# Kernel optimization log

Hardware: AMD Instinct MI355X
Metric: run time of the kernel (lower is better)

The kernel has to match this reference:

```python
import jax, jax.numpy as jnp
import numpy as np

B, T, F, D, H = 16, 512, 32, 256, 256
EPS = 1e-5


def _layernorm(y, g, b):
    m = jnp.mean(y, axis=-1, keepdims=True)
    v = jnp.mean((y - m) ** 2, axis=-1, keepdims=True)
    return (y - m) / jnp.sqrt(v + EPS) * g + b


def setup_inputs() -> dict:
    key = jax.random.key(0)
    ks = jax.random.split(key, 24)
    s = lambda fan_in: 1.0 / np.sqrt(fan_in)
    u = lambda k, shape, fan_in: jax.random.uniform(k, shape, jnp.float32, -s(fan_in), s(fan_in))
    return {
        "x": jax.random.normal(ks[0], (B, T, F), jnp.float32),
        # per-feature Linear(1, D), stacked over F
        "proj_w": u(ks[1], (F, D), 1),
        "proj_b": u(ks[2], (F, D), 1),
        # per-feature scorer GRN(D, H, 1), stacked over F
        "sc_fc1_w": u(ks[3], (F, H, D), D),
        "sc_fc1_b": u(ks[4], (F, H), D),
        "sc_fc2_w": u(ks[5], (F, 1, H), H),
        "sc_fc2_b": u(ks[6], (F, 1), H),
        "sc_gate_w": u(ks[7], (F, 1, 1), 1),
        "sc_gate_b": u(ks[8], (F, 1), 1),
        "sc_skip_w": u(ks[9], (F, 1, D), D),
        "sc_skip_b": u(ks[10], (F, 1), D),
        "sc_ln_g": jnp.ones((F, 1), jnp.float32),
        "sc_ln_b": jnp.zeros((F, 1), jnp.float32),
        # post GRN(D, H, D); in_dim == out_dim -> skip is identity
        "post_fc1_w": u(ks[11], (H, D), D),
        "post_fc1_b": u(ks[12], (H,), D),
        "post_fc2_w": u(ks[13], (D, H), H),
        "post_fc2_b": u(ks[14], (D,), H),
        "post_gate_w": u(ks[15], (D, D), D),
        "post_gate_b": u(ks[16], (D,), D),
        "post_ln_g": jnp.ones((D,), jnp.float32),
        "post_ln_b": jnp.zeros((D,), jnp.float32),
    }


def reference(x, proj_w, proj_b, sc_fc1_w, sc_fc1_b, sc_fc2_w, sc_fc2_b,
              sc_gate_w, sc_gate_b, sc_skip_w, sc_skip_b, sc_ln_g, sc_ln_b,
              post_fc1_w, post_fc1_b, post_fc2_w, post_fc2_b,
              post_gate_w, post_gate_b, post_ln_g, post_ln_b):
    # per-feature embedding: Linear(1 -> D), batched over F
    # E: [B, T, F, D]
    E = x[..., None] * proj_w[None, None] + proj_b[None, None]

    # per-feature scorer GRN(D, H, 1), all F at once
    h = jax.nn.elu(jnp.einsum("btfd,fhd->btfh", E, sc_fc1_w) + sc_fc1_b)
    h = jnp.einsum("btfh,foh->btfo", h, sc_fc2_w) + sc_fc2_b  # [B,T,F,1]
    g = jax.nn.sigmoid(jnp.einsum("btfo,fpo->btfp", h, sc_gate_w) + sc_gate_b)
    skip = jnp.einsum("btfd,fod->btfo", E, sc_skip_w) + sc_skip_b
    y = g * h + (1.0 - g) * skip
    S = _layernorm(y, sc_ln_g, sc_ln_b)  # [B,T,F,1] (last dim size 1)

    # softmax over features, weighted mixture
    W = jax.nn.softmax(S, axis=2)
    mix = jnp.sum(E * W, axis=2)  # [B,T,D]

    # post GRN(D, H, D), skip = identity
    h2 = jax.nn.elu(mix @ post_fc1_w.T + post_fc1_b)
    h2 = h2 @ post_fc2_w.T + post_fc2_b
    g2 = jax.nn.sigmoid(h2 @ post_gate_w.T + post_gate_b)
    y2 = g2 * h2 + (1.0 - g2) * mix
    return _layernorm(y2, post_ln_g, post_ln_b)
```

## Files before the change

kernel.cpp:

```cpp
#include <hip/hip_runtime.h>
#include <hip/hip_bf16.h>
#include <math.h>


typedef __bf16 bf16;
typedef __bf16 bf16x8 __attribute__((ext_vector_type(8)));
typedef __bf16 bf16x4 __attribute__((ext_vector_type(4)));
typedef float f32x4 __attribute__((ext_vector_type(4)));

#define NTOK 8192
#define D_   256
#define F_   32

#define OFF_C      512
#define OFF_WPROJT 2048
#define OFF_FC1    32768
#define OFF_FC2    163840
#define OFF_GATE   294912


__global__ __launch_bounds__(256) void vsn_prep(
    const float* __restrict__ proj_w, const float* __restrict__ proj_b,
    const float* __restrict__ sc_ln_b,
    const float* __restrict__ w1, const float* __restrict__ w2,
    const float* __restrict__ w3,
    float* __restrict__ wsC, bf16* __restrict__ wsWT,
    bf16* __restrict__ o1, bf16* __restrict__ o2, bf16* __restrict__ o3)
{
  const int blk = blockIdx.x;
  if (blk < 48) {
    int g = blk * 256 + threadIdx.x;
    int m = g >> 12;
    int c = g & 4095;
    const float* src = (m == 0) ? w1 : (m == 1) ? w2 : w3;
    bf16* dst = (m == 0) ? o1 : (m == 1) ? o2 : o3;
    int row = c >> 4, ks = (c >> 1) & 7, half = c & 1;
    int j = row >> 4, lmr = row & 15;
    const float* sp = src + row * 256 + ks * 32 + half * 16;
    bf16* dp = dst + j * 4096 + ks * 512 + lmr * 32 + half * 16;
    #pragma unroll
    for (int q = 0; q < 2; q++) {
      float4 a = ((const float4*)sp)[2 * q];
      float4 b = ((const float4*)sp)[2 * q + 1];
      bf16x8 v = {(bf16)a.x, (bf16)a.y, (bf16)a.z, (bf16)a.w,
                  (bf16)b.x, (bf16)b.y, (bf16)b.z, (bf16)b.w};
      *(bf16x8*)(dp + q * 8) = v;
    }
  } else {
    const int d = threadIdx.x;
    float wv[F_];
    float mx = -3.0e38f;
    #pragma unroll
    for (int f = 0; f < F_; f++) { wv[f] = sc_ln_b[f]; mx = fmaxf(mx, wv[f]); }
    float se = 0.0f;
    #pragma unroll
    for (int f = 0; f < F_; f++) { wv[f] = __expf(wv[f] - mx); se += wv[f]; }
    float inv = 1.0f / se;
    float acc = 0.0f;
    #pragma unroll
    for (int f = 0; f < F_; f++) {
      float wf = wv[f] * inv;
      acc += wf * proj_b[f * D_ + d];
      wsWT[d * F_ + f] = (bf16)(wf * proj_w[f * D_ + d]);
    }
    wsC[d] = acc;
  }
}

__global__ __launch_bounds__(256, 1) void vsn_main(
    const float* __restrict__ x,
    const float* __restrict__ wsC,
    const bf16* __restrict__ WT,
    const bf16* __restrict__ FC1, const float* __restrict__ fc1_b,
    const bf16* __restrict__ FC2, const float* __restrict__ fc2_b,
    const bf16* __restrict__ GATE, const float* __restrict__ gate_b,
    const float* __restrict__ ln_g, const float* __restrict__ ln_b,
    float* __restrict__ out)
{
  __shared__ bf16  sAct[2][32][264];
  __shared__ float sY[32][260];

  const int tid  = threadIdx.x;
  const int w    = tid >> 6;
  const int lane = tid & 63;
  const int lm   = lane & 15;
  const int lq   = lane >> 4;
  const int j0   = w * 4;
  const int tok0 = blockIdx.x * 32;

  bf16x4 mixh[2][4];
  {
    bf16x8 a[2];
    #pragma unroll
    for (int t = 0; t < 2; t++) {
      const float* xp = x + (size_t)(tok0 + t * 16 + lm) * F_ + lq * 8;
      float4 x0 = *(const float4*)xp;
      float4 x1 = *(const float4*)(xp + 4);
      bf16x8 av = {(bf16)x0.x, (bf16)x0.y, (bf16)x0.z, (bf16)x0.w,
                   (bf16)x1.x, (bf16)x1.y, (bf16)x1.z, (bf16)x1.w};
      a[t] = av;
    }
    #pragma unroll
    for (int jj = 0; jj < 4; jj++) {
      int n = (j0 + jj) * 16 + lm;
      bf16x8 b = *(const bf16x8*)(WT + n * F_ + lq * 8);
      float cv = wsC[n];
      #pragma unroll
      for (int t = 0; t < 2; t++) {
        f32x4 acc = {cv, cv, cv, cv};
        acc = __builtin_amdgcn_mfma_f32_16x16x32_bf16(a[t], b, acc, 0, 0, 0);
        bf16x4 mh = {(bf16)acc[0], (bf16)acc[1], (bf16)acc[2], (bf16)acc[3]};
        mixh[t][jj] = mh;
        #pragma unroll
        for (int r = 0; r < 4; r++) sAct[0][t * 16 + lq * 4 + r][n] = mh[r];
      }
    }
  }
  __syncthreads();

  auto gemmPhase = [&](int src, const bf16* __restrict__ W, auto&& epi) {
    bf16x8 af[2][8];
    #pragma unroll
    for (int t = 0; t < 2; t++)
      #pragma unroll
      for (int ks = 0; ks < 8; ks++)
        af[t][ks] = *(const bf16x8*)(&sAct[src][t * 16 + lm][ks * 32 + lq * 8]);
    const bf16* base = W + j0 * 4096 + lm * 32 + lq * 8;
    bf16x8 bb[8];
    #pragma unroll
    for (int ks = 0; ks < 8; ks++)
      bb[ks] = *(const bf16x8*)(base + ks * 512);
    #pragma unroll
    for (int jj = 0; jj < 4; jj++) {
      bf16x8 bn[8];
      if (jj < 3) {
        const bf16* nb = base + (jj + 1) * 4096;
        #pragma unroll
        for (int ks = 0; ks < 8; ks++)
          bn[ks] = *(const bf16x8*)(nb + ks * 512);
      }
      f32x4 acc0 = {0.f, 0.f, 0.f, 0.f}, acc1 = {0.f, 0.f, 0.f, 0.f};
      #pragma unroll
      for (int ks = 0; ks < 8; ks++) {
        acc0 = __builtin_amdgcn_mfma_f32_16x16x32_bf16(af[0][ks], bb[ks], acc0, 0, 0, 0);
        acc1 = __builtin_amdgcn_mfma_f32_16x16x32_bf16(af[1][ks], bb[ks], acc1, 0, 0, 0);
      }
      epi(jj, acc0, acc1);
      if (jj < 3) {
        #pragma unroll
        for (int ks = 0; ks < 8; ks++) bb[ks] = bn[ks];
      }
    }
  };

  gemmPhase(0, FC1, [&](int jj, f32x4& a0, f32x4& a1) {
    int n = (j0 + jj) * 16 + lm;
    float bias = fc1_b[n];
    #pragma unroll
    for (int r = 0; r < 4; r++) {
      float v0 = a0[r] + bias;
      v0 = (v0 > 0.0f) ? v0 : (__expf(v0) - 1.0f);
      sAct[1][lq * 4 + r][n] = (bf16)v0;
      float v1 = a1[r] + bias;
      v1 = (v1 > 0.0f) ? v1 : (__expf(v1) - 1.0f);
      sAct[1][16 + lq * 4 + r][n] = (bf16)v1;
    }
  });
  __syncthreads();

  bf16x4 h2h[2][4];
  gemmPhase(1, FC2, [&](int jj, f32x4& a0, f32x4& a1) {
    int n = (j0 + jj) * 16 + lm;
    float bias = fc2_b[n];
    bf16x4 h0, h1v;
    #pragma unroll
    for (int r = 0; r < 4; r++) {
      h0[r]  = (bf16)(a0[r] + bias);
      h1v[r] = (bf16)(a1[r] + bias);
      sAct[0][lq * 4 + r][n] = h0[r];
      sAct[0][16 + lq * 4 + r][n] = h1v[r];
    }
    h2h[0][jj] = h0;
    h2h[1][jj] = h1v;
  });
  __syncthreads();

  gemmPhase(0, GATE, [&](int jj, f32x4& a0, f32x4& a1) {
    int n = (j0 + jj) * 16 + lm;
    float bias = gate_b[n];
    #pragma unroll
    for (int r = 0; r < 4; r++) {
      float s0 = a0[r] + bias;
      float g0 = 1.0f / (1.0f + __expf(-s0));
      sY[lq * 4 + r][n] = g0 * (float)h2h[0][jj][r] + (1.0f - g0) * (float)mixh[0][jj][r];
      float s1 = a1[r] + bias;
      float g1 = 1.0f / (1.0f + __expf(-s1));
      sY[16 + lq * 4 + r][n] = g1 * (float)h2h[1][jj][r] + (1.0f - g1) * (float)mixh[1][jj][r];
    }
  });
  __syncthreads();

  const float inv_d = 1.0f / 256.0f;
  #pragma unroll
  for (int rep = 0; rep < 2; rep++) {
    const int t = (w * 4 + lq) * 2 + rep;
    float4 yv[4];
    #pragma unroll
    for (int i = 0; i < 4; i++)
      yv[i] = *(const float4*)(&sY[t][lm * 4 + i * 64]);
    float s = 0.0f;
    #pragma unroll
    for (int i = 0; i < 4; i++) s += yv[i].x + yv[i].y + yv[i].z + yv[i].w;
    #pragma unroll
    for (int off = 1; off < 16; off <<= 1) s += __shfl_xor(s, off);
    float mean = s * inv_d;
    float q = 0.0f;
    #pragma unroll
    for (int i = 0; i < 4; i++) {
      float d0 = yv[i].x - mean, d1 = yv[i].y - mean,
            d2 = yv[i].z - mean, d3 = yv[i].w - mean;
      q += d0 * d0 + d1 * d1 + d2 * d2 + d3 * d3;
    }
    #pragma unroll
    for (int off = 1; off < 16; off <<= 1) q += __shfl_xor(q, off);
    float rstd = rsqrtf(q * inv_d + 1e-5f);
    #pragma unroll
    for (int i = 0; i < 4; i++) {
      int n = lm * 4 + i * 64;
      float4 gv = *(const float4*)(ln_g + n);
      float4 bv = *(const float4*)(ln_b + n);
      float4 o;
      o.x = (yv[i].x - mean) * rstd * gv.x + bv.x;
      o.y = (yv[i].y - mean) * rstd * gv.y + bv.y;
      o.z = (yv[i].z - mean) * rstd * gv.z + bv.z;
      o.w = (yv[i].w - mean) * rstd * gv.w + bv.w;
      *(float4*)(out + (size_t)(tok0 + t) * D_ + n) = o;
    }
  }
}

extern "C" void kernel_launch(void* const* d_in, const int* in_sizes, int n_in,
                              void* d_out, int out_size, void* d_ws, size_t ws_size,
                              hipStream_t stream) {
  (void)in_sizes; (void)n_in; (void)ws_size; (void)out_size;
  const float* x      = (const float*)d_in[0];
  const float* proj_w = (const float*)d_in[1];
  const float* proj_b = (const float*)d_in[2];
  const float* sclnb  = (const float*)d_in[12];
  const float* fc1w   = (const float*)d_in[13];
  const float* fc1b   = (const float*)d_in[14];
  const float* fc2w   = (const float*)d_in[15];
  const float* fc2b   = (const float*)d_in[16];
  const float* gw     = (const float*)d_in[17];
  const float* gb     = (const float*)d_in[18];
  const float* lng    = (const float*)d_in[19];
  const float* lnb    = (const float*)d_in[20];

  char* ws = (char*)d_ws;
  float* wsC   = (float*)(ws + OFF_C);
  bf16*  wsWT  = (bf16*)(ws + OFF_WPROJT);
  bf16*  bFC1  = (bf16*)(ws + OFF_FC1);
  bf16*  bFC2  = (bf16*)(ws + OFF_FC2);
  bf16*  bGATE = (bf16*)(ws + OFF_GATE);

  vsn_prep<<<49, 256, 0, stream>>>(proj_w, proj_b, sclnb, fc1w, fc2w, gw,
                                   wsC, wsWT, bFC1, bFC2, bGATE);
  vsn_main<<<NTOK / 32, 256, 0, stream>>>(x, wsC, wsWT,
                                          bFC1, fc1b, bFC2, fc2b, bGATE, gb,
                                          lng, lnb, (float*)d_out);
}
```

Baseline: 110.6 us.

## Fuse weight prep into main kernel, read fp32 weights and convert on the fly

Removes the separate prep kernel and its workspace round trip. Each block now recomputes the softmax-weighted projection table in shared memory, and the GEMM phases load fp32 weights straight from global memory and convert them to bf16 in registers. This saves one launch and the prep-to-main dependency, but each block does redundant prep work and GEMM weight loads double in bytes, with register pressure rising from the fp32 prefetch buffers.

```diff
diff --git a/kernel.cpp b/kernel.cpp
--- a/kernel.cpp
+++ b/kernel.cpp
@@ -12,73 +12,26 @@
 #define D_   256
 #define F_   32
 
-#define OFF_C      512
-#define OFF_WPROJT 2048
-#define OFF_FC1    32768
-#define OFF_FC2    163840
-#define OFF_GATE   294912
-
-
-__global__ __launch_bounds__(256) void vsn_prep(
+static __device__ inline bf16x8 cvt8(float4 a, float4 b) {
+  bf16x8 v = {(bf16)a.x, (bf16)a.y, (bf16)a.z, (bf16)a.w,
+              (bf16)b.x, (bf16)b.y, (bf16)b.z, (bf16)b.w};
+  return v;
+}
+
+__global__ __launch_bounds__(256, 1) void vsn_fused(
+    const float* __restrict__ x,
     const float* __restrict__ proj_w, const float* __restrict__ proj_b,
     const float* __restrict__ sc_ln_b,
-    const float* __restrict__ w1, const float* __restrict__ w2,
-    const float* __restrict__ w3,
-    float* __restrict__ wsC, bf16* __restrict__ wsWT,
-    bf16* __restrict__ o1, bf16* __restrict__ o2, bf16* __restrict__ o3)
-{
-  const int blk = blockIdx.x;
-  if (blk < 48) {
-    int g = blk * 256 + threadIdx.x;
-    int m = g >> 12;
-    int c = g & 4095;
-    const float* src = (m == 0) ? w1 : (m == 1) ? w2 : w3;
-    bf16* dst = (m == 0) ? o1 : (m == 1) ? o2 : o3;
-    int row = c >> 4, ks = (c >> 1) & 7, half = c & 1;
-    int j = row >> 4, lmr = row & 15;
-    const float* sp = src + row * 256 + ks * 32 + half * 16;
-    bf16* dp = dst + j * 4096 + ks * 512 + lmr * 32 + half * 16;
-    #pragma unroll
-    for (int q = 0; q < 2; q++) {
-      float4 a = ((const float4*)sp)[2 * q];
-      float4 b = ((const float4*)sp)[2 * q + 1];
-      bf16x8 v = {(bf16)a.x, (bf16)a.y, (bf16)a.z, (bf16)a.w,
-                  (bf16)b.x, (bf16)b.y, (bf16)b.z, (bf16)b.w};
-      *(bf16x8*)(dp + q * 8) = v;
-    }
-  } else {
-    const int d = threadIdx.x;
-    float wv[F_];
-    float mx = -3.0e38f;
-    #pragma unroll
-    for (int f = 0; f < F_; f++) { wv[f] = sc_ln_b[f]; mx = fmaxf(mx, wv[f]); }
-    float se = 0.0f;
-    #pragma unroll
-    for (int f = 0; f < F_; f++) { wv[f] = __expf(wv[f] - mx); se += wv[f]; }
-    float inv = 1.0f / se;
-    float acc = 0.0f;
-    #pragma unroll
-    for (int f = 0; f < F_; f++) {
-      float wf = wv[f] * inv;
-      acc += wf * proj_b[f * D_ + d];
-      wsWT[d * F_ + f] = (bf16)(wf * proj_w[f * D_ + d]);
-    }
-    wsC[d] = acc;
-  }
-}
-
-__global__ __launch_bounds__(256, 1) void vsn_main(
-    const float* __restrict__ x,
-    const float* __restrict__ wsC,
-    const bf16* __restrict__ WT,
-    const bf16* __restrict__ FC1, const float* __restrict__ fc1_b,
-    const bf16* __restrict__ FC2, const float* __restrict__ fc2_b,
-    const bf16* __restrict__ GATE, const float* __restrict__ gate_b,
+    const float* __restrict__ FC1, const float* __restrict__ fc1_b,
+    const float* __restrict__ FC2, const float* __restrict__ fc2_b,
+    const float* __restrict__ GATE, const float* __restrict__ gate_b,
     const float* __restrict__ ln_g, const float* __restrict__ ln_b,
     float* __restrict__ out)
 {
-  __shared__ bf16  sAct[2][32][264];
-  __shared__ float sY[32][260];
+  __shared__ __align__(16) bf16  sWT[256][40];
+  __shared__ float sC[256];
+  __shared__ __align__(16) bf16  sAct[2][32][264];
+  __shared__ __align__(16) float sY[32][260];
 
   const int tid  = threadIdx.x;
   const int w    = tid >> 6;
@@ -88,6 +41,34 @@
   const int j0   = w * 4;
   const int tok0 = blockIdx.x * 32;
 
+  {
+    float wv[F_];
+    float mx = -3.0e38f;
+    #pragma unroll
+    for (int f = 0; f < F_; f++) { wv[f] = sc_ln_b[f]; mx = fmaxf(mx, wv[f]); }
+    float se = 0.0f;
+    #pragma unroll
+    for (int f = 0; f < F_; f++) { wv[f] = __expf(wv[f] - mx); se += wv[f]; }
+    const float inv = 1.0f / se;
+
+    const int d = tid;
+    float acc = 0.0f;
+    #pragma unroll
+    for (int q = 0; q < 4; q++) {
+      bf16x8 v;
+      #pragma unroll
+      for (int e = 0; e < 8; e++) {
+        int f = q * 8 + e;
+        float wf = wv[f] * inv;
+        acc += wf * proj_b[f * D_ + d];
+        v[e] = (bf16)(wf * proj_w[f * D_ + d]);
+      }
+      *(bf16x8*)(&sWT[d][q * 8]) = v;
+    }
+    sC[d] = acc;
+  }
+  __syncthreads();
+
   bf16x4 mixh[2][4];
   {
     bf16x8 a[2];
@@ -96,15 +77,13 @@
       const float* xp = x + (size_t)(tok0 + t * 16 + lm) * F_ + lq * 8;
       float4 x0 = *(const float4*)xp;
       float4 x1 = *(const float4*)(xp + 4);
-      bf16x8 av = {(bf16)x0.x, (bf16)x0.y, (bf16)x0.z, (bf16)x0.w,
-                   (bf16)x1.x, (bf16)x1.y, (bf16)x1.z, (bf16)x1.w};
-      a[t] = av;
+      a[t] = cvt8(x0, x1);
     }
     #pragma unroll
     for (int jj = 0; jj < 4; jj++) {
       int n = (j0 + jj) * 16 + lm;
-      bf16x8 b = *(const bf16x8*)(WT + n * F_ + lq * 8);
-      float cv = wsC[n];
+      bf16x8 b = *(const bf16x8*)(&sWT[n][lq * 8]);
+      float cv = sC[n];
       #pragma unroll
       for (int t = 0; t < 2; t++) {
         f32x4 acc = {cv, cv, cv, cv};
@@ -118,26 +97,31 @@
   }
   __syncthreads();
 
-  auto gemmPhase = [&](int src, const bf16* __restrict__ W, auto&& epi) {
+  auto gemmPhase = [&](int src, const float* __restrict__ W, auto&& epi) {
     bf16x8 af[2][8];
     #pragma unroll
     for (int t = 0; t < 2; t++)
       #pragma unroll
       for (int ks = 0; ks < 8; ks++)
         af[t][ks] = *(const bf16x8*)(&sAct[src][t * 16 + lm][ks * 32 + lq * 8]);
-    const bf16* base = W + j0 * 4096 + lm * 32 + lq * 8;
+    const float* base = W + (size_t)(j0 * 16 + lm) * D_ + lq * 8;
     bf16x8 bb[8];
     #pragma unroll
-    for (int ks = 0; ks < 8; ks++)
-      bb[ks] = *(const bf16x8*)(base + ks * 512);
+    for (int ks = 0; ks < 8; ks++) {
+      float4 p0 = *(const float4*)(base + ks * 32);
+      float4 p1 = *(const float4*)(base + ks * 32 + 4);
+      bb[ks] = cvt8(p0, p1);
+    }
     #pragma unroll
     for (int jj = 0; jj < 4; jj++) {
-      bf16x8 bn[8];
+      float4 na[8], nb[8];
       if (jj < 3) {
-        const bf16* nb = base + (jj + 1) * 4096;
+        const float* nbp = base + (size_t)(jj + 1) * 16 * D_;
         #pragma unroll
-        for (int ks = 0; ks < 8; ks++)
-          bn[ks] = *(const bf16x8*)(nb + ks * 512);
+        for (int ks = 0; ks < 8; ks++) {
+          na[ks] = *(const float4*)(nbp + ks * 32);
+          nb[ks] = *(const float4*)(nbp + ks * 32 + 4);
+        }
       }
       f32x4 acc0 = {0.f, 0.f, 0.f, 0.f}, acc1 = {0.f, 0.f, 0.f, 0.f};
       #pragma unroll
@@ -148,7 +132,7 @@
       epi(jj, acc0, acc1);
       if (jj < 3) {
         #pragma unroll
-        for (int ks = 0; ks < 8; ks++) bb[ks] = bn[ks];
+        for (int ks = 0; ks < 8; ks++) bb[ks] = cvt8(na[ks], nb[ks]);
       }
     }
   };
@@ -242,7 +226,7 @@
 extern "C" void kernel_launch(void* const* d_in, const int* in_sizes, int n_in,
                               void* d_out, int out_size, void* d_ws, size_t ws_size,
                               hipStream_t stream) {
-  (void)in_sizes; (void)n_in; (void)ws_size; (void)out_size;
+  (void)in_sizes; (void)n_in; (void)ws_size; (void)out_size; (void)d_ws;
   const float* x      = (const float*)d_in[0];
   const float* proj_w = (const float*)d_in[1];
   const float* proj_b = (const float*)d_in[2];
@@ -256,16 +240,7 @@
   const float* lng    = (const float*)d_in[19];
   const float* lnb    = (const float*)d_in[20];
 
-  char* ws = (char*)d_ws;
-  float* wsC   = (float*)(ws + OFF_C);
-  bf16*  wsWT  = (bf16*)(ws + OFF_WPROJT);
-  bf16*  bFC1  = (bf16*)(ws + OFF_FC1);
-  bf16*  bFC2  = (bf16*)(ws + OFF_FC2);
-  bf16*  bGATE = (bf16*)(ws + OFF_GATE);
-
-  vsn_prep<<<49, 256, 0, stream>>>(proj_w, proj_b, sclnb, fc1w, fc2w, gw,
-                                   wsC, wsWT, bFC1, bFC2, bGATE);
-  vsn_main<<<NTOK / 32, 256, 0, stream>>>(x, wsC, wsWT,
-                                          bFC1, fc1b, bFC2, fc2b, bGATE, gb,
-                                          lng, lnb, (float*)d_out);
+  vsn_fused<<<NTOK / 32, 256, 0, stream>>>(x, proj_w, proj_b, sclnb,
+                                           fc1w, fc1b, fc2w, fc2b, gw, gb,
+                                           lng, lnb, (float*)d_out);
 }
```

Result: slower. 124.3 us (+12.3%).

## Fuse prep and main kernels into one cooperative launch with grid sync

Applied to the files above, without the earlier changes.

Merges the weight-conversion prep kernel and the main fused VSN kernel into a single cooperative kernel. The first 49 blocks perform the prep work, then all 256 blocks hit a grid-wide barrier before running the main computation. This removes a kernel launch and the inter-kernel gap, at the cost of a grid sync and cooperative launch overhead. It also requires all 256 blocks (one per CU at launch bounds 256,1) to be co-resident.

```diff
diff --git a/kernel.cpp b/kernel.cpp
--- a/kernel.cpp
+++ b/kernel.cpp
@@ -1,6 +1,9 @@
 #include <hip/hip_runtime.h>
+#include <hip/hip_cooperative_groups.h>
 #include <hip/hip_bf16.h>
 #include <math.h>
+
+namespace cg = cooperative_groups;
 
 
 typedef __bf16 bf16;
@@ -19,17 +22,26 @@
 #define OFF_GATE   294912
 
 
-__global__ __launch_bounds__(256) void vsn_prep(
+__global__ __launch_bounds__(256, 1) void vsn_coop(
+    const float* __restrict__ x,
     const float* __restrict__ proj_w, const float* __restrict__ proj_b,
     const float* __restrict__ sc_ln_b,
-    const float* __restrict__ w1, const float* __restrict__ w2,
-    const float* __restrict__ w3,
+    const float* __restrict__ w1, const float* __restrict__ fc1_b,
+    const float* __restrict__ w2, const float* __restrict__ fc2_b,
+    const float* __restrict__ w3, const float* __restrict__ gate_b,
+    const float* __restrict__ ln_g, const float* __restrict__ ln_b,
     float* __restrict__ wsC, bf16* __restrict__ wsWT,
-    bf16* __restrict__ o1, bf16* __restrict__ o2, bf16* __restrict__ o3)
+    bf16* __restrict__ o1, bf16* __restrict__ o2, bf16* __restrict__ o3,
+    float* __restrict__ out)
 {
+  __shared__ bf16  sAct[2][32][264];
+  __shared__ float sY[32][260];
+
+  const int tid = threadIdx.x;
   const int blk = blockIdx.x;
+
   if (blk < 48) {
-    int g = blk * 256 + threadIdx.x;
+    int g = blk * 256 + tid;
     int m = g >> 12;
     int c = g & 4095;
     const float* src = (m == 0) ? w1 : (m == 1) ? w2 : w3;
@@ -46,8 +58,8 @@
                   (bf16)b.x, (bf16)b.y, (bf16)b.z, (bf16)b.w};
       *(bf16x8*)(dp + q * 8) = v;
     }
-  } else {
-    const int d = threadIdx.x;
+  } else if (blk == 48) {
+    const int d = tid;
     float wv[F_];
     float mx = -3.0e38f;
     #pragma unroll
@@ -65,28 +77,21 @@
     }
     wsC[d] = acc;
   }
-}
-
-__global__ __launch_bounds__(256, 1) void vsn_main(
-    const float* __restrict__ x,
-    const float* __restrict__ wsC,
-    const bf16* __restrict__ WT,
-    const bf16* __restrict__ FC1, const float* __restrict__ fc1_b,
-    const bf16* __restrict__ FC2, const float* __restrict__ fc2_b,
-    const bf16* __restrict__ GATE, const float* __restrict__ gate_b,
-    const float* __restrict__ ln_g, const float* __restrict__ ln_b,
-    float* __restrict__ out)
-{
-  __shared__ bf16  sAct[2][32][264];
-  __shared__ float sY[32][260];
-
-  const int tid  = threadIdx.x;
+
+  __threadfence();
+  cg::this_grid().sync();
+
   const int w    = tid >> 6;
   const int lane = tid & 63;
   const int lm   = lane & 15;
   const int lq   = lane >> 4;
   const int j0   = w * 4;
-  const int tok0 = blockIdx.x * 32;
+  const int tok0 = blk * 32;
+
+  const bf16* WT   = wsWT;
+  const bf16* FC1  = o1;
+  const bf16* FC2  = o2;
+  const bf16* GATE = o3;
 
   bf16x4 mixh[2][4];
   {
@@ -262,10 +267,15 @@
   bf16*  bFC1  = (bf16*)(ws + OFF_FC1);
   bf16*  bFC2  = (bf16*)(ws + OFF_FC2);
   bf16*  bGATE = (bf16*)(ws + OFF_GATE);
-
-  vsn_prep<<<49, 256, 0, stream>>>(proj_w, proj_b, sclnb, fc1w, fc2w, gw,
-                                   wsC, wsWT, bFC1, bFC2, bGATE);
-  vsn_main<<<NTOK / 32, 256, 0, stream>>>(x, wsC, wsWT,
-                                          bFC1, fc1b, bFC2, fc2b, bGATE, gb,
-                                          lng, lnb, (float*)d_out);
+  float* outp  = (float*)d_out;
+
+  void* args[] = {
+    (void*)&x, (void*)&proj_w, (void*)&proj_b, (void*)&sclnb,
+    (void*)&fc1w, (void*)&fc1b, (void*)&fc2w, (void*)&fc2b,
+    (void*)&gw, (void*)&gb, (void*)&lng, (void*)&lnb,
+    (void*)&wsC, (void*)&wsWT, (void*)&bFC1, (void*)&bFC2, (void*)&bGATE,
+    (void*)&outp
+  };
+  hipLaunchCooperativeKernel((void*)vsn_coop, dim3(NTOK / 32), dim3(256),
+                             args, 0, stream);
 }
```

New measurement: 184.4 us. 1.67x slower.
